# Performance work log

Measured on AMD Instinct MI355X. Metric: run time of the kernel, lower is better.

## Reference

```python
import jax, jax.numpy as jnp
import numpy as np

B, C, HIMG, WIMG = 32, 3, 224, 224
P, D, L, F, H, NC = 16, 768, 12, 3072, 12, 1000
S = (HIMG // P) * (WIMG // P)  # 196 tokens
DH = D // H                    # 64 per head


def setup_inputs() -> dict:
    key = jax.random.key(0)
    ks = jax.random.split(key, 12)
    rn = lambda i, shape, sc: jax.random.normal(ks[i], shape, jnp.float32) * sc
    return dict(
        x=rn(0, (B, C, HIMG, WIMG), 1.0),
        conv_w=rn(1, (D, C, P, P), 0.02),
        conv_b=jnp.zeros((D,), jnp.float32),
        pos_embed=rn(2, (S, D), 0.02),
        ln1_s=jnp.ones((L, D), jnp.float32),
        ln1_b=jnp.zeros((L, D), jnp.float32),
        wq=rn(3, (L, D, D), 0.02),
        wk=rn(4, (L, D, D), 0.02),
        wv=rn(5, (L, D, D), 0.02),
        ln2_s=jnp.ones((L, D), jnp.float32),
        ln2_b=jnp.zeros((L, D), jnp.float32),
        w1=rn(6, (L, D, F), 0.02),
        b1=jnp.zeros((L, F), jnp.float32),
        w2=rn(7, (L, F, D), 0.02),
        b2=jnp.zeros((L, D), jnp.float32),
        fc_w=rn(8, (D, NC), 0.02),
        fc_b=jnp.zeros((NC,), jnp.float32),
    )


def _layernorm(x, scale, bias, eps=1e-5):
    m = x.mean(-1, keepdims=True)
    v = ((x - m) ** 2).mean(-1, keepdims=True)
    return (x - m) * jax.lax.rsqrt(v + eps) * scale + bias


def reference(x, conv_w, conv_b, pos_embed, ln1_s, ln1_b, wq, wk, wv,
              ln2_s, ln2_b, w1, b1, w2, b2, fc_w, fc_b):
    # patch embedding: stride-P conv, then b c h w -> b (h w) c, add pos embed
    h = jax.lax.conv_general_dilated(
        x, conv_w, (P, P), 'VALID',
        dimension_numbers=('NCHW', 'OIHW', 'NCHW'))
    h = h + conv_b[None, :, None, None]
    h = h.reshape(B, D, S).transpose(0, 2, 1) + pos_embed  # [B,S,D]

    # NOTE: original scales attention logits by 1/sqrt(seq_len), not 1/sqrt(d_head)
    scale = 1.0 / jnp.sqrt(jnp.float32(S))

    def layer(hx, p):
        l1s, l1b, Wq, Wk, Wv, l2s, l2b, W1, B1, W2, B2 = p
        xn = _layernorm(hx, l1s, l1b)
        q = (xn @ Wq).reshape(B, S, H, DH)
        k = (xn @ Wk).reshape(B, S, H, DH)
        v = (xn @ Wv).reshape(B, S, H, DH)
        att = jax.nn.softmax(jnp.einsum('bshd,bthd->bhst', q, k) * scale, axis=-1)
        o = jnp.einsum('bhst,bthd->bshd', att, v).reshape(B, S, D)
        hx = hx + o
        y = _layernorm(hx, l2s, l2b) @ W1 + B1
        y = jax.nn.gelu(y, approximate=False) @ W2 + B2
        return hx + y, None

    h, _ = jax.lax.scan(layer, h, (ln1_s, ln1_b, wq, wk, wv,
                                   ln2_s, ln2_b, w1, b1, w2, b2))
    return h.mean(axis=1) @ fc_w + fc_b  # [B, num_classes]
```

## Files before the change

### kernel.cpp

```cpp
#include <hip/hip_runtime.h>
#include <hip/hip_bf16.h>

typedef __attribute__((ext_vector_type(8))) short bf16x8;
typedef __attribute__((ext_vector_type(4))) short bf16x4;
typedef __attribute__((ext_vector_type(4))) float f32x4;

#define DEVI static __device__ __forceinline__

DEVI unsigned short f2bf(float f) {
  __hip_bfloat16 h = __float2bfloat16(f);
  return __builtin_bit_cast(unsigned short, h);
}

DEVI f32x4 mfma16(bf16x8 a, bf16x8 b, f32x4 c) {
  return __builtin_amdgcn_mfma_f32_16x16x32_bf16(a, b, c, 0, 0, 0);
}

DEVI void gload16(const unsigned short* g, unsigned short* l) {
  __builtin_amdgcn_global_load_lds(
      (const __attribute__((address_space(1))) void*)g,
      (__attribute__((address_space(3))) void*)l, 16, 0, 0);
}

DEVI float erf_fast(float x) {
  float ax = fabsf(x);
  float t = 1.f / (1.f + 0.3275911f * ax);
  float poly = ((((1.061405429f * t - 1.453152027f) * t + 1.421413741f) * t -
                 0.284496736f) * t + 0.254829592f) * t;
  float e = __expf(-x * x);
  float er = 1.f - poly * e;
  return copysignf(er, x);
}

__global__ __launch_bounds__(256) void k_im2col(const float* __restrict__ x,
                                                unsigned short* __restrict__ A) {
  int t = blockIdx.x * 256 + threadIdx.x;
  int m = t / 192;
  int qq = t - m * 192;
  int kk = qq * 4;
  int c = kk >> 8;
  int r = kk & 255;
  int i = r >> 4;
  int j = r & 15;
  int b = m / 196;
  int s = m - b * 196;
  int ph = s / 14;
  int pw = s - ph * 14;
  const float* src = x + ((size_t)((b * 3 + c) * 224 + ph * 16 + i)) * 224 + pw * 16 + j;
  f32x4 v = *reinterpret_cast<const f32x4*>(src);
  bf16x4 o;
  o[0] = (short)f2bf(v[0]); o[1] = (short)f2bf(v[1]);
  o[2] = (short)f2bf(v[2]); o[3] = (short)f2bf(v[3]);
  *reinterpret_cast<bf16x4*>(A + (size_t)m * 768 + kk) = o;
}

__global__ __launch_bounds__(256) void k_cvt(const float* __restrict__ in,
                                             unsigned short* __restrict__ out) {
  int t = blockIdx.x * 256 + threadIdx.x;
  f32x4 v = *reinterpret_cast<const f32x4*>(in + (size_t)t * 4);
  bf16x4 o;
  o[0] = (short)f2bf(v[0]); o[1] = (short)f2bf(v[1]);
  o[2] = (short)f2bf(v[2]); o[3] = (short)f2bf(v[3]);
  *reinterpret_cast<bf16x4*>(out + (size_t)t * 4) = o;
}

DEVI void transpose_tile(const float* __restrict__ in, unsigned short* __restrict__ out,
                         int K, int N, int kt, int nt, unsigned short (*tile)[68]) {
  int r = threadIdx.x >> 4;
  int c4 = (threadIdx.x & 15) * 4;
  int k0 = kt * 64, n0 = nt * 64;
#pragma unroll
  for (int rr0 = 0; rr0 < 4; rr0++) {
    int rr = r + rr0 * 16;
    f32x4 v = *reinterpret_cast<const f32x4*>(in + (size_t)(k0 + rr) * N + n0 + c4);
    bf16x4 o;
    o[0] = (short)f2bf(v[0]); o[1] = (short)f2bf(v[1]);
    o[2] = (short)f2bf(v[2]); o[3] = (short)f2bf(v[3]);
    *reinterpret_cast<bf16x4*>(&tile[rr][c4]) = o;
  }
  __syncthreads();
#pragma unroll
  for (int rr0 = 0; rr0 < 4; rr0++) {
    int rr = r + rr0 * 16;
    bf16x4 o;
    o[0] = (short)tile[c4 + 0][rr];
    o[1] = (short)tile[c4 + 1][rr];
    o[2] = (short)tile[c4 + 2][rr];
    o[3] = (short)tile[c4 + 3][rr];
    *reinterpret_cast<bf16x4*>(out + (size_t)(n0 + rr) * K + k0 + c4) = o;
  }
}

__global__ __launch_bounds__(256) void k_wconvert(
    const float* __restrict__ wq, const float* __restrict__ wk, const float* __restrict__ wv,
    const float* __restrict__ w1, const float* __restrict__ w2,
    unsigned short* __restrict__ wqkvT, unsigned short* __restrict__ w1T,
    unsigned short* __restrict__ w2T) {
  __shared__ unsigned short tile[64][68];
  int bid = blockIdx.x;
  if (bid < 432) {
    int mm = bid / 144, t2 = bid - mm * 144;
    const float* in = (mm == 0) ? wq : ((mm == 1) ? wk : wv);
    transpose_tile(in, wqkvT + (size_t)mm * 768 * 768, 768, 768, t2 / 12, t2 % 12, tile);
  } else if (bid < 1008) {
    int t2 = bid - 432;
    transpose_tile(w1, w1T, 768, 3072, t2 / 48, t2 % 48, tile);
  } else {
    int t2 = bid - 1008;
    transpose_tile(w2, w2T, 3072, 768, t2 / 12, t2 % 12, tile);
  }
}

__global__ __launch_bounds__(256) void k_ln(const float* __restrict__ h,
                                            const float* __restrict__ sc,
                                            const float* __restrict__ bi,
                                            unsigned short* __restrict__ xn) {
  int wave = threadIdx.x >> 6, lane = threadIdx.x & 63;
  int row = blockIdx.x * 4 + wave;
  const float* hr = h + (size_t)row * 768;
  f32x4 v[3];
  float sum = 0.f;
#pragma unroll
  for (int i = 0; i < 3; i++) {
    v[i] = *reinterpret_cast<const f32x4*>(hr + i * 256 + lane * 4);
    sum += v[i][0] + v[i][1] + v[i][2] + v[i][3];
  }
#pragma unroll
  for (int m = 1; m < 64; m <<= 1) sum += __shfl_xor(sum, m, 64);
  float mean = sum * (1.f / 768.f);
  float var = 0.f;
#pragma unroll
  for (int i = 0; i < 3; i++)
#pragma unroll
    for (int c = 0; c < 4; c++) { float d = v[i][c] - mean; var += d * d; }
#pragma unroll
  for (int m = 1; m < 64; m <<= 1) var += __shfl_xor(var, m, 64);
  float rs = rsqrtf(var * (1.f / 768.f) + 1e-5f);
#pragma unroll
  for (int i = 0; i < 3; i++) {
    int col = i * 256 + lane * 4;
    f32x4 s4 = *reinterpret_cast<const f32x4*>(sc + col);
    f32x4 b4 = *reinterpret_cast<const f32x4*>(bi + col);
    bf16x4 o;
#pragma unroll
    for (int c = 0; c < 4; c++) o[c] = (short)f2bf((v[i][c] - mean) * rs * s4[c] + b4[c]);
    *reinterpret_cast<bf16x4*>(xn + (size_t)row * 768 + col) = o;
  }
}

template <int EPI>
__global__ __launch_bounds__(256) void k_gemm(
    const unsigned short* __restrict__ A, const unsigned short* __restrict__ Bt, int K,
    const float* __restrict__ bias, const float* __restrict__ aux,
    float* __restrict__ outF, unsigned short* __restrict__ outB) {
  __shared__ __align__(16) unsigned short As[2][128 * 32];
  __shared__ __align__(16) unsigned short Bs[2][128 * 32];

  int GX = gridDim.x, GY = gridDim.y;
  int nb = GX * GY;
  int lin = blockIdx.y * GX + blockIdx.x;
  int q = nb >> 3, r8 = nb & 7;
  int xcd = lin & 7, off = lin >> 3;
  int wid = (xcd < r8 ? xcd * (q + 1) : r8 * (q + 1) + (xcd - r8) * q) + off;
  const int GM = 8;
  int per = GM * GX;
  int g = wid / per;
  int first_m = g * GM;
  int gm = min(GM, GY - first_m);
  int rem = wid - g * per;
  int mt = first_m + rem % gm;
  int nt = rem / gm;
  int m0 = mt * 128, n0 = nt * 128;

  int tid = threadIdx.x;
  int wave = tid >> 6, lane = tid & 63;
  int wm = (wave >> 1) * 64, wn = (wave & 1) * 64;
  int lr = lane & 15, lg = lane >> 4;

  f32x4 acc[4][4];
  const f32x4 fz = {0.f, 0.f, 0.f, 0.f};
#pragma unroll
  for (int i = 0; i < 4; i++)
#pragma unroll
    for (int j = 0; j < 4; j++) acc[i][j] = fz;

  int srow = wave * 16 + (lane >> 2);
  int scol = (lane & 3) * 8;
  const unsigned short* Ag = A + (size_t)(m0 + srow) * K + scol;
  const unsigned short* Bg = Bt + (size_t)(n0 + srow) * K + scol;
  int lofs = wave * 16 * 32;

  int nk = K >> 5;
#pragma unroll
  for (int j = 0; j < 2; j++) {
    gload16(Ag + (size_t)j * 64 * K, &As[0][lofs + j * 64 * 32]);
    gload16(Bg + (size_t)j * 64 * K, &Bs[0][lofs + j * 64 * 32]);
  }
  __syncthreads();

  for (int kt = 0; kt < nk - 1; kt++) {
    int cur = kt & 1;
    int k0 = (kt + 1) << 5;
#pragma unroll
    for (int j = 0; j < 2; j++) {
      gload16(Ag + (size_t)j * 64 * K + k0, &As[cur ^ 1][lofs + j * 64 * 32]);
      gload16(Bg + (size_t)j * 64 * K + k0, &Bs[cur ^ 1][lofs + j * 64 * 32]);
    }
    bf16x8 a[4], b[4];
#pragma unroll
    for (int i = 0; i < 4; i++) {
      a[i] = *reinterpret_cast<const bf16x8*>(&As[cur][(wm + i * 16 + lr) * 32 + lg * 8]);
      b[i] = *reinterpret_cast<const bf16x8*>(&Bs[cur][(wn + i * 16 + lr) * 32 + lg * 8]);
    }
#pragma unroll
    for (int mi = 0; mi < 4; mi++)
#pragma unroll
      for (int ni = 0; ni < 4; ni++) acc[mi][ni] = mfma16(a[mi], b[ni], acc[mi][ni]);
    __syncthreads();
  }
  {
    int cur = (nk - 1) & 1;
    bf16x8 a[4], b[4];
#pragma unroll
    for (int i = 0; i < 4; i++) {
      a[i] = *reinterpret_cast<const bf16x8*>(&As[cur][(wm + i * 16 + lr) * 32 + lg * 8]);
      b[i] = *reinterpret_cast<const bf16x8*>(&Bs[cur][(wn + i * 16 + lr) * 32 + lg * 8]);
    }
#pragma unroll
    for (int mi = 0; mi < 4; mi++)
#pragma unroll
      for (int ni = 0; ni < 4; ni++) acc[mi][ni] = mfma16(a[mi], b[ni], acc[mi][ni]);
  }

#pragma unroll
  for (int mi = 0; mi < 4; mi++) {
    int mb = m0 + wm + mi * 16 + lg * 4;
    int bb = mb / 196;
    int s0 = mb - bb * 196;
#pragma unroll
    for (int ni = 0; ni < 4; ni++) {
      int n = n0 + wn + ni * 16 + lr;
      int s = s0;
#pragma unroll
      for (int r = 0; r < 4; r++) {
        int m = mb + r;
        float val = acc[mi][ni][r];
        if (EPI == 0) {
          outF[(size_t)m * 768 + n] = val + bias[n] + aux[(size_t)s * 768 + n];
          s++;
          if (s == 196) s = 0;
        } else {
          outF[(size_t)m * 768 + n] += val + bias[n];
        }
      }
    }
  }
}

template <int EPI>
__global__ __launch_bounds__(512, 2) void k_gemm256p(
    const unsigned short* __restrict__ A, const unsigned short* __restrict__ Bt,
    const float* __restrict__ bias, unsigned short* __restrict__ outB) {
  const int K = 768, NK = 24;
  __shared__ __align__(16) unsigned short LDS[4][16384];
  const int MVALID = 6272;

  int GX = gridDim.x, GY = gridDim.y;
  int nb = GX * GY;
  int lin = blockIdx.y * GX + blockIdx.x;
  int q = nb >> 3, r8 = nb & 7;
  int xcd = lin & 7, off = lin >> 3;
  int wid = (xcd < r8 ? xcd * (q + 1) : r8 * (q + 1) + (xcd - r8) * q) + off;
  const int GM = 4;
  int per = GM * GX;
  int g = wid / per;
  int first_m = g * GM;
  int gm = min(GM, GY - first_m);
  int rem = wid - g * per;
  int mt = first_m + rem % gm;
  int nt = rem / gm;
  int m0 = mt * 256, n0 = nt * 256;

  int tid = threadIdx.x;
  int w = tid >> 6, lane = tid & 63;
  int wm = w >> 2, wn = w & 3;
  int lr = lane & 15, lg = lane >> 4;

  f32x4 acc[8][4];
  const f32x4 fz = {0.f, 0.f, 0.f, 0.f};
#pragma unroll
  for (int i = 0; i < 8; i++)
#pragma unroll
    for (int j = 0; j < 4; j++) acc[i][j] = fz;

  int srow = w * 16 + (lane >> 2);
  int scol = ((lane & 3) ^ ((lane >> 3) & 3)) * 8;
  const unsigned short* Ag = A + (size_t)(m0 + srow) * K + scol;
  const unsigned short* Bg = Bt + (size_t)(n0 + srow) * K + scol;
  int ldst = w * 512;

  int colsw = (lg ^ ((lr >> 1) & 3)) * 8;
  int rofA = wm * 4096 + lr * 32 + colsw;
  int rofB = 8192 + wn * 2048 + lr * 32 + colsw;

#define STAGEP(kt)                                                          \
  {                                                                         \
    unsigned short* d_ = &LDS[(kt) & 3][0];                                 \
    const unsigned short* a_ = Ag + (kt) * 32;                              \
    const unsigned short* b_ = Bg + (kt) * 32;                              \
    gload16(a_, d_ + ldst);                                                 \
    gload16(a_ + (size_t)128 * K, d_ + 4096 + ldst);                        \
    gload16(b_, d_ + 8192 + ldst);                                          \
    gload16(b_ + (size_t)128 * K, d_ + 12288 + ldst);                       \
  }

  STAGEP(0);
  STAGEP(1);
  STAGEP(2);
  asm volatile("s_waitcnt vmcnt(8)" ::: "memory");
  __builtin_amdgcn_s_barrier();

  for (int kt = 0; kt < NK; kt++) {
    if (kt + 3 < NK) STAGEP(kt + 3);
    const unsigned short* bufA = &LDS[kt & 3][0];
    bf16x8 a[8], b[4];
#pragma unroll
    for (int ni = 0; ni < 4; ni++)
      b[ni] = *reinterpret_cast<const bf16x8*>(bufA + rofB + ni * 512);
#pragma unroll
    for (int mi = 0; mi < 8; mi++)
      a[mi] = *reinterpret_cast<const bf16x8*>(bufA + rofA + mi * 512);
    __builtin_amdgcn_s_setprio(1);
#pragma unroll
    for (int mi = 0; mi < 8; mi++)
#pragma unroll
      for (int ni = 0; ni < 4; ni++) acc[mi][ni] = mfma16(a[mi], b[ni], acc[mi][ni]);
    __builtin_amdgcn_s_setprio(0);
    if (kt + 1 < NK) {
      asm volatile("s_waitcnt lgkmcnt(0)" ::: "memory");
      if (kt + 3 < NK) {
        asm volatile("s_waitcnt vmcnt(8)" ::: "memory");
      } else if (kt + 2 < NK) {
        asm volatile("s_waitcnt vmcnt(4)" ::: "memory");
      } else {
        asm volatile("s_waitcnt vmcnt(0)" ::: "memory");
      }
      __builtin_amdgcn_s_barrier();
    }
  }
#undef STAGEP

  if (EPI == 1) {
#pragma unroll
    for (int ni = 0; ni < 4; ni++) {
      int n = n0 + wn * 64 + ni * 16 + lr;
      int which = (n >= 1536) ? 2 : ((n >= 768) ? 1 : 0);
      int n7 = n - which * 768;
      int hd = n7 >> 6, dh = n7 & 63;
      unsigned short* ob = outB + (size_t)which * 4816896 + dh;
#pragma unroll
      for (int mi = 0; mi < 8; mi++) {
        int mb = m0 + wm * 128 + mi * 16 + lg * 4;
        if (mb >= MVALID) continue;
        int bb = mb / 196;
        int s = mb - bb * 196;
#pragma unroll
        for (int r = 0; r < 4; r++) {
          ob[((size_t)((bb * 12 + hd) * 196 + s) << 6)] = f2bf(acc[mi][ni][r]);
          s++;
          if (s == 196) { s = 0; bb++; }
        }
      }
    }
  } else {
#pragma unroll
    for (int mi = 0; mi < 8; mi++) {
      int mb = m0 + wm * 128 + mi * 16 + lg * 4;
      if (mb >= MVALID) continue;
#pragma unroll
      for (int ni = 0; ni < 4; ni++) {
        int n = n0 + wn * 64 + ni * 16 + lr;
#pragma unroll
        for (int r = 0; r < 4; r++) {
          int m = mb + r;
          float u = acc[mi][ni][r] + bias[n];
          float gg = 0.5f * u * (1.f + erf_fast(u * 0.70710678118654752f));
          outB[(size_t)m * 3072 + n] = f2bf(gg);
        }
      }
    }
  }
}

__global__ __launch_bounds__(256) void k_attn(const unsigned short* __restrict__ q,
                                              const unsigned short* __restrict__ k,
                                              const unsigned short* __restrict__ v,
                                              float* __restrict__ h) {
  __shared__ __align__(16) unsigned short Kl[208][72];
  __shared__ __align__(16) unsigned short Vt[64][248];
  __shared__ __align__(16) unsigned short Sc[4][16][232];
  int bh = blockIdx.x;
  int b = bh / 12, hh = bh - b * 12;
  size_t base = (size_t)bh * 196 * 64;
  int tid = threadIdx.x, wave = tid >> 6, lane = tid & 63;
  int lr = lane & 15, lg = lane >> 4;

  const bf16x8 bz = {0, 0, 0, 0, 0, 0, 0, 0};
  for (int u = tid; u < 208 * 8; u += 256) {
    int row = u >> 3, c8 = (u & 7) * 8;
    bf16x8 val = bz;
    if (row < 196) val = *reinterpret_cast<const bf16x8*>(k + base + row * 64 + c8);
    *reinterpret_cast<bf16x8*>(&Kl[row][c8]) = val;
  }
  for (int u = tid; u < 224 * 8; u += 256) {
    int t = u >> 3, d8 = (u & 7) * 8;
    bf16x8 val = bz;
    if (t < 196) val = *reinterpret_cast<const bf16x8*>(v + base + t * 64 + d8);
#pragma unroll
    for (int i = 0; i < 8; i++) Vt[d8 + i][t] = (unsigned short)val[i];
  }
  for (int i2 = lane; i2 < 256; i2 += 64) Sc[wave][i2 >> 4][208 + (i2 & 15)] = 0;
  __syncthreads();

  const float scale = 1.f / 14.f;
  for (int st = wave; st < 13; st += 4) {
    int qb = st * 16;
    int s = qb + lr;
    bf16x8 aq0 = bz, aq1 = bz;
    if (s < 196) {
      aq0 = *reinterpret_cast<const bf16x8*>(q + base + (size_t)s * 64 + lg * 8);
      aq1 = *reinterpret_cast<const bf16x8*>(q + base + (size_t)s * 64 + 32 + lg * 8);
    }
    f32x4 sc[13];
#pragma unroll
    for (int t = 0; t < 13; t++) {
      bf16x8 bk0 = *reinterpret_cast<const bf16x8*>(&Kl[t * 16 + lr][lg * 8]);
      bf16x8 bk1 = *reinterpret_cast<const bf16x8*>(&Kl[t * 16 + lr][32 + lg * 8]);
      f32x4 z = {0.f, 0.f, 0.f, 0.f};
      z = mfma16(aq0, bk0, z);
      z = mfma16(aq1, bk1, z);
      sc[t] = z;
    }
    float mx[4] = {-1e30f, -1e30f, -1e30f, -1e30f};
#pragma unroll
    for (int t = 0; t < 13; t++) {
      int tc = t * 16 + lr;
#pragma unroll
      for (int r = 0; r < 4; r++) {
        float xv = (tc < 196) ? sc[t][r] * scale : -1e30f;
        sc[t][r] = xv;
        mx[r] = fmaxf(mx[r], xv);
      }
    }
#pragma unroll
    for (int r = 0; r < 4; r++)
#pragma unroll
      for (int mm = 1; mm < 16; mm <<= 1) mx[r] = fmaxf(mx[r], __shfl_xor(mx[r], mm, 64));
    float sm[4] = {0.f, 0.f, 0.f, 0.f};
#pragma unroll
    for (int t = 0; t < 13; t++)
#pragma unroll
      for (int r = 0; r < 4; r++) {
        float e = __expf(sc[t][r] - mx[r]);
        sc[t][r] = e;
        sm[r] += e;
      }
#pragma unroll
    for (int r = 0; r < 4; r++)
#pragma unroll
      for (int mm = 1; mm < 16; mm <<= 1) sm[r] += __shfl_xor(sm[r], mm, 64);
    float inv[4];
#pragma unroll
    for (int r = 0; r < 4; r++) inv[r] = 1.f / sm[r];
#pragma unroll
    for (int t = 0; t < 13; t++)
#pragma unroll
      for (int r = 0; r < 4; r++)
        Sc[wave][lg * 4 + r][t * 16 + lr] = f2bf(sc[t][r] * inv[r]);
    asm volatile("s_waitcnt lgkmcnt(0)" ::: "memory");
    bf16x8 ap[7];
#pragma unroll
    for (int ks = 0; ks < 7; ks++)
      ap[ks] = *reinterpret_cast<const bf16x8*>(&Sc[wave][lr][ks * 32 + lg * 8]);
#pragma unroll
    for (int nt = 0; nt < 4; nt++) {
      f32x4 o = {0.f, 0.f, 0.f, 0.f};
#pragma unroll
      for (int ks = 0; ks < 7; ks++) {
        bf16x8 bv = *reinterpret_cast<const bf16x8*>(&Vt[nt * 16 + lr][ks * 32 + lg * 8]);
        o = mfma16(ap[ks], bv, o);
      }
#pragma unroll
      for (int r = 0; r < 4; r++) {
        int s2 = qb + lg * 4 + r;
        if (s2 < 196) h[(size_t)(b * 196 + s2) * 768 + hh * 64 + nt * 16 + lr] += o[r];
      }
    }
  }
}

__global__ __launch_bounds__(256) void k_mean(const float* __restrict__ h,
                                              float* __restrict__ hm) {
  int b = blockIdx.x, d = blockIdx.y * 256 + threadIdx.x;
  float acc = 0.f;
  for (int s = 0; s < 196; s++) acc += h[(size_t)(b * 196 + s) * 768 + d];
  hm[b * 768 + d] = acc * (1.f / 196.f);
}

__global__ __launch_bounds__(256) void k_fc(const float* __restrict__ hm,
                                            const float* __restrict__ w,
                                            const float* __restrict__ bias,
                                            float* __restrict__ out) {
  int b = blockIdx.x, n = blockIdx.y * 256 + threadIdx.x;
  if (n >= 1000) return;
  float acc = bias[n];
  for (int d = 0; d < 768; d++) acc += hm[b * 768 + d] * w[d * 1000 + n];
  out[b * 1000 + n] = acc;
}

extern "C" void kernel_launch(void* const* d_in, const int* in_sizes, int n_in,
                              void* d_out, int out_size, void* d_ws, size_t ws_size,
                              hipStream_t stream) {
  const float* x      = (const float*)d_in[0];
  const float* conv_w = (const float*)d_in[1];
  const float* conv_b = (const float*)d_in[2];
  const float* pos    = (const float*)d_in[3];
  const float* ln1_s  = (const float*)d_in[4];
  const float* ln1_b  = (const float*)d_in[5];
  const float* wq     = (const float*)d_in[6];
  const float* wk     = (const float*)d_in[7];
  const float* wv     = (const float*)d_in[8];
  const float* ln2_s  = (const float*)d_in[9];
  const float* ln2_b  = (const float*)d_in[10];
  const float* w1     = (const float*)d_in[11];
  const float* b1     = (const float*)d_in[12];
  const float* w2     = (const float*)d_in[13];
  const float* b2     = (const float*)d_in[14];
  const float* fc_w   = (const float*)d_in[15];
  const float* fc_b   = (const float*)d_in[16];
  float* out = (float*)d_out;

  char* p = (char*)d_ws;
  auto alloc = [&](size_t bytes) {
    char* r = p;
    p += (bytes + 255) & ~(size_t)255;
    return r;
  };
  const size_t M = 6272, MP = 6400, QSZ = 4816896;
  float* h              = (float*)alloc(M * 768 * 4);
  unsigned short* xn    = (unsigned short*)alloc(MP * 768 * 2);
  unsigned short* qkv   = (unsigned short*)alloc(3 * QSZ * 2);
  unsigned short* y1    = (unsigned short*)alloc(MP * 3072 * 2);
  unsigned short* wqkvT = (unsigned short*)alloc((size_t)2304 * 768 * 2);
  unsigned short* w1T   = (unsigned short*)alloc((size_t)3072 * 768 * 2);
  unsigned short* w2T   = (unsigned short*)alloc((size_t)3072 * 768 * 2);
  float* hm             = (float*)alloc(32 * 768 * 4);
  unsigned short* cwB   = qkv;

  k_cvt<<<576, 256, 0, stream>>>(conv_w, cwB);
  k_im2col<<<4704, 256, 0, stream>>>(x, xn);
  k_gemm<0><<<dim3(6, 49), 256, 0, stream>>>(xn, cwB, 768, conv_b, pos, h, nullptr);

  for (int l = 0; l < 12; l++) {
    k_wconvert<<<1584, 256, 0, stream>>>(
        wq + (size_t)l * 589824, wk + (size_t)l * 589824, wv + (size_t)l * 589824,
        w1 + (size_t)l * 2359296, w2 + (size_t)l * 2359296, wqkvT, w1T, w2T);
    k_ln<<<1568, 256, 0, stream>>>(h, ln1_s + l * 768, ln1_b + l * 768, xn);
    k_gemm256p<1><<<dim3(9, 25), 512, 0, stream>>>(xn, wqkvT, nullptr, qkv);
    k_attn<<<384, 256, 0, stream>>>(qkv, qkv + QSZ, qkv + 2 * QSZ, h);
    k_ln<<<1568, 256, 0, stream>>>(h, ln2_s + l * 768, ln2_b + l * 768, xn);
    k_gemm256p<2><<<dim3(12, 25), 512, 0, stream>>>(xn, w1T, b1 + (size_t)l * 3072, y1);
    k_gemm<3><<<dim3(6, 49), 256, 0, stream>>>(y1, w2T, 3072, b2 + (size_t)l * 768, nullptr,
                                               h, nullptr);
  }
  k_mean<<<dim3(32, 3), 256, 0, stream>>>(h, hm);
  k_fc<<<dim3(32, 4), 256, 0, stream>>>(hm, fc_w, fc_b, out);
}
```

Measured before the change: 3.266 ms.

## Split GEMM k-tile into two half-phases interleaving loads and MFMAs

Restructures the main GEMM k-loop into two phases per tile: half the B fragments feed MFMAs while the A-half of the next stage's global-to-LDS loads is issued, then the other half. An extra barrier sits between the phases, and sched_barrier pins instruction order. The goal is to interleave memory issue with matrix work, lower register pressure on B fragments, and peel the tail iterations so the waitcnt values are constants. Each tile now carries an additional barrier, and the forced ordering may limit what the compiler can schedule.

```diff
diff --git a/kernel.cpp b/kernel.cpp
--- a/kernel.cpp
+++ b/kernel.cpp
@@ -303,52 +303,71 @@
   int rofA = wm * 4096 + lr * 32 + colsw;
   int rofB = 8192 + wn * 2048 + lr * 32 + colsw;
 
-#define STAGEP(kt)                                                          \
+#define STAGEA(kt)                                                          \
   {                                                                         \
     unsigned short* d_ = &LDS[(kt) & 3][0];                                 \
     const unsigned short* a_ = Ag + (kt) * 32;                              \
-    const unsigned short* b_ = Bg + (kt) * 32;                              \
     gload16(a_, d_ + ldst);                                                 \
     gload16(a_ + (size_t)128 * K, d_ + 4096 + ldst);                        \
+  }
+#define STAGEB(kt)                                                          \
+  {                                                                         \
+    unsigned short* d_ = &LDS[(kt) & 3][0];                                 \
+    const unsigned short* b_ = Bg + (kt) * 32;                              \
     gload16(b_, d_ + 8192 + ldst);                                          \
     gload16(b_ + (size_t)128 * K, d_ + 12288 + ldst);                       \
   }
 
-  STAGEP(0);
-  STAGEP(1);
-  STAGEP(2);
+#define KTILE(ktv, VMSTR, STG, LAST)                                         \
+  {                                                                          \
+    const int kt_ = (ktv);                                                   \
+    const unsigned short* buf_ = &LDS[kt_ & 3][0];                           \
+    bf16x8 afr[8], bfr[2];                                                   \
+                \
+    _Pragma("unroll") for (int mi = 0; mi < 8; mi++) afr[mi] =               \
+        *reinterpret_cast<const bf16x8*>(buf_ + rofA + mi * 512);            \
+    _Pragma("unroll") for (int ni = 0; ni < 2; ni++) bfr[ni] =               \
+        *reinterpret_cast<const bf16x8*>(buf_ + rofB + ni * 512);            \
+    if (STG) STAGEA(kt_ + 3);                                                \
+    asm volatile("s_waitcnt lgkmcnt(0)" ::: "memory");                       \
+    __builtin_amdgcn_sched_barrier(0);                                       \
+    __builtin_amdgcn_s_setprio(1);                                           \
+    _Pragma("unroll") for (int mi = 0; mi < 8; mi++)                         \
+        _Pragma("unroll") for (int ni = 0; ni < 2; ni++)                     \
+            acc[mi][ni] = mfma16(afr[mi], bfr[ni], acc[mi][ni]);             \
+    __builtin_amdgcn_s_setprio(0);                                           \
+    __builtin_amdgcn_s_barrier();               \
+                       \
+    _Pragma("unroll") for (int ni = 0; ni < 2; ni++) bfr[ni] =               \
+        *reinterpret_cast<const bf16x8*>(buf_ + rofB + (2 + ni) * 512);      \
+    if (STG) STAGEB(kt_ + 3);                                                \
+    asm volatile("s_waitcnt lgkmcnt(0)" ::: "memory");                       \
+    __builtin_amdgcn_sched_barrier(0);                                       \
+    __builtin_amdgcn_s_setprio(1);                                           \
+    _Pragma("unroll") for (int mi = 0; mi < 8; mi++)                         \
+        _Pragma("unroll") for (int ni = 0; ni < 2; ni++)                     \
+            acc[mi][2 + ni] = mfma16(afr[mi], bfr[ni], acc[mi][2 + ni]);     \
+    __builtin_amdgcn_s_setprio(0);                                           \
+    if (!LAST) {                                                             \
+        \
+      asm volatile("s_waitcnt vmcnt(" VMSTR ")" ::: "memory");               \
+      __builtin_amdgcn_s_barrier();                                          \
+    }                                                                        \
+  }
+
+  STAGEA(0); STAGEB(0);
+  STAGEA(1); STAGEB(1);
+  STAGEA(2); STAGEB(2);
   asm volatile("s_waitcnt vmcnt(8)" ::: "memory");
   __builtin_amdgcn_s_barrier();
 
-  for (int kt = 0; kt < NK; kt++) {
-    if (kt + 3 < NK) STAGEP(kt + 3);
-    const unsigned short* bufA = &LDS[kt & 3][0];
-    bf16x8 a[8], b[4];
-#pragma unroll
-    for (int ni = 0; ni < 4; ni++)
-      b[ni] = *reinterpret_cast<const bf16x8*>(bufA + rofB + ni * 512);
-#pragma unroll
-    for (int mi = 0; mi < 8; mi++)
-      a[mi] = *reinterpret_cast<const bf16x8*>(bufA + rofA + mi * 512);
-    __builtin_amdgcn_s_setprio(1);
-#pragma unroll
-    for (int mi = 0; mi < 8; mi++)
-#pragma unroll
-      for (int ni = 0; ni < 4; ni++) acc[mi][ni] = mfma16(a[mi], b[ni], acc[mi][ni]);
-    __builtin_amdgcn_s_setprio(0);
-    if (kt + 1 < NK) {
-      asm volatile("s_waitcnt lgkmcnt(0)" ::: "memory");
-      if (kt + 3 < NK) {
-        asm volatile("s_waitcnt vmcnt(8)" ::: "memory");
-      } else if (kt + 2 < NK) {
-        asm volatile("s_waitcnt vmcnt(4)" ::: "memory");
-      } else {
-        asm volatile("s_waitcnt vmcnt(0)" ::: "memory");
-      }
-      __builtin_amdgcn_s_barrier();
-    }
-  }
-#undef STAGEP
+  for (int kt = 0; kt < NK - 3; kt++) KTILE(kt, "8", true, false);
+  KTILE(NK - 3, "4", false, false);
+  KTILE(NK - 2, "0", false, false);
+  KTILE(NK - 1, "0", false, true);
+#undef KTILE
+#undef STAGEA
+#undef STAGEB
 
   if (EPI == 1) {
 #pragma unroll
```

Result: no change. 3.228 ms (-1.2%).
